# Performance work log

Hardware: AMD Instinct MI355X
Metric: run time of the kernel (lower is better)

## Reference

```python
import jax, jax.numpy as jnp
import numpy as np

N = 50000      # num_nodes
E = 800000     # num_edges (before self-loops)
IN = 512       # in_channels
HID = 64       # hidden_channels
H = 8          # num_heads (layer 1)
OUT = 128      # out_channels
NEG_SLOPE = 0.2


def setup_inputs() -> dict:
    key = jax.random.key(0)
    ks = jax.random.split(key, 10)
    x = jax.random.normal(ks[0], (N, IN), jnp.float32)
    edge_index = jax.random.randint(ks[1], (2, E), 0, N, jnp.int32)

    def glorot(k, shape):
        fan_in, fan_out = shape[0], int(np.prod(shape[1:]))
        s = jnp.sqrt(2.0 / (fan_in + fan_out)).astype(jnp.float32)
        return jax.random.normal(k, shape, jnp.float32) * s

    # layer 1: GATConv(IN -> HID, heads=H, concat=True)
    W1 = glorot(ks[2], (IN, H * HID))
    att_src1 = glorot(ks[3], (H, HID))
    att_dst1 = glorot(ks[4], (H, HID))
    b1 = jnp.zeros((H * HID,), jnp.float32)
    # layer 2: GATConv(H*HID -> OUT, heads=1, concat=False)
    W2 = glorot(ks[5], (H * HID, OUT))
    att_src2 = glorot(ks[6], (1, OUT))
    att_dst2 = glorot(ks[7], (1, OUT))
    b2 = jnp.zeros((OUT,), jnp.float32)
    return {"x": x, "edge_index": edge_index,
            "W1": W1, "b1": b1, "att_src1": att_src1, "att_dst1": att_dst1,
            "W2": W2, "b2": b2, "att_src2": att_src2, "att_dst2": att_dst2}


def gat_layer(x, src, dst, W, b, a_src, a_dst, heads, concat):
    n = x.shape[0]
    h = (x @ W).reshape(n, heads, -1)                     # [N, H, C]
    e_src = (h * a_src).sum(-1)                           # [N, H]
    e_dst = (h * a_dst).sum(-1)                           # [N, H]
    e = jax.nn.leaky_relu(e_src[src] + e_dst[dst], NEG_SLOPE)   # [E, H]
    # segment softmax over incoming edges of each destination node
    m = jax.ops.segment_max(e, dst, num_segments=n)       # [N, H]
    m = jnp.where(jnp.isneginf(m), 0.0, m)                # empty segments
    p = jnp.exp(e - m[dst])                               # [E, H]
    s = jax.ops.segment_sum(p, dst, num_segments=n)       # [N, H]
    alpha = p / (s[dst] + 1e-16)                          # [E, H]
    out = jax.ops.segment_sum(alpha[..., None] * h[src], dst, num_segments=n)  # [N, H, C]
    if concat:
        return out.reshape(n, -1) + b
    return out.mean(axis=1) + b


def reference(x, edge_index, W1, b1, att_src1, att_dst1, W2, b2, att_src2, att_dst2):
    # PyG GATConv adds self-loops by default
    loops = jnp.arange(N, dtype=edge_index.dtype)
    src = jnp.concatenate([edge_index[0], loops])
    dst = jnp.concatenate([edge_index[1], loops])
    h = gat_layer(x, src, dst, W1, b1, att_src1, att_dst1, H, True)   # [N, H*HID]
    h = jax.nn.relu(h)
    out = gat_layer(h, src, dst, W2, b2, att_src2, att_dst2, 1, False)  # [N, OUT]
    return out
```

## Files before the change

### kernel.cpp

```cpp
#include <hip/hip_runtime.h>

#define NNODES 50000
#define NEDGES 800000
#define ETOT   (NNODES + NEDGES)
#define NH     8
#define HID    64
#define D1     512
#define INC    512
#define OUTC   128
#define NEG    0.2f
#define MPAD   50048

typedef __attribute__((ext_vector_type(8))) short short8;
typedef __attribute__((ext_vector_type(4))) float f32x4;

__device__ __forceinline__ float bf2f(ushort u) { return __uint_as_float(((uint)u) << 16); }
__device__ __forceinline__ ushort f2bf(float x) {
    uint u = __float_as_uint(x);
    u += 0x7fffu + ((u >> 16) & 1u);
    return (ushort)(u >> 16);
}
__device__ __forceinline__ float leaky(float v) { return v >= 0.f ? v : NEG * v; }
__device__ __forceinline__ unsigned fkey(float v) {
    unsigned u = __float_as_uint(v);
    return (u & 0x80000000u) ? ~u : (u | 0x80000000u);
}
__device__ __forceinline__ float funkey(unsigned k) {
    return __uint_as_float((k & 0x80000000u) ? (k & 0x7fffffffu) : ~k);
}

__global__ void count_deg(const int* __restrict__ ei, int* __restrict__ deg) {
    int i = blockIdx.x * 256 + threadIdx.x;
    if (i >= ETOT) return;
    int dst = (i < NEDGES) ? ei[NEDGES + i] : (i - NEDGES);
    atomicAdd(&deg[dst], 1);
}

__global__ void scan_deg(const int* __restrict__ deg, int* __restrict__ rs) {
    __shared__ int part[1024];
    const int n = NNODES;
    const int CH = (n + 1023) / 1024;
    int t = threadIdx.x;
    int lo = t * CH, hi = min(lo + CH, n);
    int s = 0;
    for (int i = lo; i < hi; ++i) s += deg[i];
    part[t] = s;
    __syncthreads();
    for (int off = 1; off < 1024; off <<= 1) {
        int v = (t >= off) ? part[t - off] : 0;
        __syncthreads();
        part[t] += v;
        __syncthreads();
    }
    int run = (t == 0) ? 0 : part[t - 1];
    for (int i = lo; i < hi; ++i) { rs[i] = run; run += deg[i]; }
    if (hi == n) rs[n] = run;
}

__global__ void scatter_edges(const int* __restrict__ ei, int* __restrict__ cursor,
                              int* __restrict__ csr_src) {
    int i = blockIdx.x * 256 + threadIdx.x;
    if (i >= ETOT) return;
    int src, dst;
    if (i < NEDGES) { src = ei[i]; dst = ei[NEDGES + i]; }
    else            { src = dst = i - NEDGES; }
    int pos = atomicAdd(&cursor[dst], 1);
    csr_src[pos] = src;
}

__global__ void cast_bf16(const float* __restrict__ x, ushort* __restrict__ xb, int n4) {
    int i = blockIdx.x * 256 + threadIdx.x;
    if (i >= n4) return;
    float4 v = *(const float4*)&x[(size_t)i * 4];
    ushort4 o = { f2bf(v.x), f2bf(v.y), f2bf(v.z), f2bf(v.w) };
    *(ushort4*)&xb[(size_t)i * 4] = o;
}

__global__ void cast_wT(const float* __restrict__ W, ushort* __restrict__ WT, int K, int N) {
    int idx = blockIdx.x * 256 + threadIdx.x;
    if (idx >= K * N) return;
    int n = idx / K, k = idx - n * K;
    WT[idx] = f2bf(W[(size_t)k * N + n]);
}

template<int KDIM>
__global__ __launch_bounds__(256) void gemm_bf16(const ushort* __restrict__ A,
                                                 const ushort* __restrict__ Bt,
                                                 ushort* __restrict__ C,
                                                 int M, int N) {
    __shared__ __align__(16) ushort Asl[128 * 64];
    __shared__ __align__(16) ushort Bsl[128 * 64];
    const int tid  = threadIdx.x;
    const int lane = tid & 63;
    const int wid  = tid >> 6;
    const int wr   = wid >> 1, wc = wid & 1;
    const int fr   = lane & 15, fq = lane >> 4;
    const int m0   = blockIdx.x * 128;
    const int n0   = blockIdx.y * 128;

    f32x4 acc[4][4] = {};

    for (int k0 = 0; k0 < KDIM; k0 += 64) {
        __syncthreads();
        #pragma unroll
        for (int i = 0; i < 4; ++i) {
            int chunk = wid * 4 + i;
            int r = chunk * 8 + (lane >> 3);
            const ushort* ga = A  + (size_t)(m0 + r) * KDIM + k0 + (lane & 7) * 8;
            const ushort* gb = Bt + (size_t)(n0 + r) * KDIM + k0 + (lane & 7) * 8;
            __builtin_amdgcn_global_load_lds(
                (const __attribute__((address_space(1))) void*)ga,
                (__attribute__((address_space(3))) void*)(Asl + chunk * 512), 16, 0, 0);
            __builtin_amdgcn_global_load_lds(
                (const __attribute__((address_space(1))) void*)gb,
                (__attribute__((address_space(3))) void*)(Bsl + chunk * 512), 16, 0, 0);
        }
        __syncthreads();
        #pragma unroll
        for (int ks = 0; ks < 2; ++ks) {
            short8 a[4], b[4];
            #pragma unroll
            for (int m = 0; m < 4; ++m)
                a[m] = *(const short8*)&Asl[(wr * 64 + m * 16 + fr) * 64 + ks * 32 + fq * 8];
            #pragma unroll
            for (int n = 0; n < 4; ++n)
                b[n] = *(const short8*)&Bsl[(wc * 64 + n * 16 + fr) * 64 + ks * 32 + fq * 8];
            #pragma unroll
            for (int m = 0; m < 4; ++m)
                #pragma unroll
                for (int n = 0; n < 4; ++n)
                    acc[m][n] = __builtin_amdgcn_mfma_f32_16x16x32_bf16(a[m], b[n], acc[m][n], 0, 0, 0);
        }
    }
    #pragma unroll
    for (int m = 0; m < 4; ++m) {
        #pragma unroll
        for (int r = 0; r < 4; ++r) {
            int row = m0 + wr * 64 + m * 16 + fq * 4 + r;
            if (row >= M) continue;
            #pragma unroll
            for (int n = 0; n < 4; ++n)
                C[(size_t)row * N + n0 + wc * 64 + n * 16 + fr] = f2bf(acc[m][n][r]);
        }
    }
}

__global__ void dots1(const ushort* __restrict__ h1, const float* __restrict__ a_src,
                      const float* __restrict__ a_dst,
                      float* __restrict__ es, float* __restrict__ ed) {
    int gw   = (blockIdx.x * blockDim.x + threadIdx.x) >> 6;
    int lane = threadIdx.x & 63;
    if (gw >= NNODES) return;
    short8 v = *(const short8*)&h1[(size_t)gw * D1 + lane * 8];
    int h = lane >> 3, c0 = (lane & 7) * 8;
    float s = 0.f, d = 0.f;
    #pragma unroll
    for (int j = 0; j < 8; ++j) {
        float x = bf2f((ushort)v[j]);
        s += x * a_src[h * HID + c0 + j];
        d += x * a_dst[h * HID + c0 + j];
    }
    #pragma unroll
    for (int off = 1; off < 8; off <<= 1) {
        s += __shfl_xor(s, off);
        d += __shfl_xor(d, off);
    }
    if ((lane & 7) == 0) { es[gw * NH + h] = s; ed[gw * NH + h] = d; }
}

__global__ void dots2(const ushort* __restrict__ h2, const float* __restrict__ a_src,
                      const float* __restrict__ a_dst,
                      float* __restrict__ es, float* __restrict__ ed) {
    int gw   = (blockIdx.x * blockDim.x + threadIdx.x) >> 6;
    int lane = threadIdx.x & 63;
    if (gw >= NNODES) return;
    uint u = *(const uint*)&h2[(size_t)gw * OUTC + lane * 2];
    float x0 = bf2f((ushort)(u & 0xffffu)), x1 = bf2f((ushort)(u >> 16));
    float s = x0 * a_src[lane * 2] + x1 * a_src[lane * 2 + 1];
    float d = x0 * a_dst[lane * 2] + x1 * a_dst[lane * 2 + 1];
    #pragma unroll
    for (int off = 1; off < 64; off <<= 1) {
        s += __shfl_xor(s, off);
        d += __shfl_xor(d, off);
    }
    if (lane == 0) { es[gw] = s; ed[gw] = d; }
}

#define CAP1 128
__global__ __launch_bounds__(256) void attn1(const ushort* __restrict__ h1,
                                             const float* __restrict__ esrc,
                                             const float* __restrict__ edst,
                                             const int* __restrict__ rs,
                                             const int* __restrict__ csr_src,
                                             const float* __restrict__ b1,
                                             ushort* __restrict__ out1) {
    int n = blockIdx.x;
    int t = threadIdx.x;
    int beg = rs[n], deg = rs[n + 1] - beg;
    __shared__ float alpha_sh[CAP1][NH];
    __shared__ unsigned mkey[NH];
    __shared__ float msh[NH], ssh[NH], rinv[NH];
    if (t < NH) { mkey[t] = 0u; ssh[t] = 0.f; }
    __syncthreads();
    for (int idx = t; idx < deg * NH; idx += 256) {
        int e = idx >> 3, h = idx & 7;
        int s = csr_src[beg + e];
        float v = leaky(esrc[s * NH + h] + edst[n * NH + h]);
        atomicMax(&mkey[h], fkey(v));
        if (e < CAP1) alpha_sh[e][h] = v;
    }
    __syncthreads();
    if (t < NH) msh[t] = funkey(mkey[t]);
    __syncthreads();
    for (int idx = t; idx < deg * NH; idx += 256) {
        int e = idx >> 3, h = idx & 7;
        float v;
        if (e < CAP1) v = alpha_sh[e][h];
        else {
            int s = csr_src[beg + e];
            v = leaky(esrc[s * NH + h] + edst[n * NH + h]);
        }
        float p = __expf(v - msh[h]);
        atomicAdd(&ssh[h], p);
        if (e < CAP1) alpha_sh[e][h] = p;
    }
    __syncthreads();
    if (t < NH) rinv[t] = 1.f / (ssh[t] + 1e-16f);
    __syncthreads();
    int c0 = 2 * t;
    int h = t >> 5;
    float m = msh[h], ri = rinv[h], edn = edst[n * NH + h];
    float acc0 = 0.f, acc1 = 0.f;
    for (int e = 0; e < deg; ++e) {
        int s = csr_src[beg + e];
        float a;
        if (e < CAP1) a = alpha_sh[e][h];
        else          a = __expf(leaky(esrc[s * NH + h] + edn) - m);
        uint u = *(const uint*)&h1[(size_t)s * D1 + c0];
        acc0 += a * bf2f((ushort)(u & 0xffffu));
        acc1 += a * bf2f((ushort)(u >> 16));
    }
    float o0 = fmaxf(acc0 * ri + b1[c0], 0.f);
    float o1 = fmaxf(acc1 * ri + b1[c0 + 1], 0.f);
    uint pk = (uint)f2bf(o0) | ((uint)f2bf(o1) << 16);
    *(uint*)&out1[(size_t)n * D1 + c0] = pk;
}

#define CAP2 128
__global__ __launch_bounds__(128) void attn2(const ushort* __restrict__ h2,
                                             const float* __restrict__ esrc,
                                             const float* __restrict__ edst,
                                             const int* __restrict__ rs,
                                             const int* __restrict__ csr_src,
                                             const float* __restrict__ b2,
                                             float* __restrict__ out) {
    int n = blockIdx.x;
    int t = threadIdx.x;
    int beg = rs[n], deg = rs[n + 1] - beg;
    __shared__ float alpha_sh[CAP2];
    __shared__ unsigned mkey;
    __shared__ float msh, ssh, rinv;
    if (t == 0) { mkey = 0u; ssh = 0.f; }
    __syncthreads();
    float edn = edst[n];
    for (int e = t; e < deg; e += 128) {
        int s = csr_src[beg + e];
        float v = leaky(esrc[s] + edn);
        atomicMax(&mkey, fkey(v));
        if (e < CAP2) alpha_sh[e] = v;
    }
    __syncthreads();
    if (t == 0) msh = funkey(mkey);
    __syncthreads();
    for (int e = t; e < deg; e += 128) {
        float v;
        if (e < CAP2) v = alpha_sh[e];
        else { int s = csr_src[beg + e]; v = leaky(esrc[s] + edn); }
        float p = __expf(v - msh);
        atomicAdd(&ssh, p);
        if (e < CAP2) alpha_sh[e] = p;
    }
    __syncthreads();
    if (t == 0) rinv = 1.f / (ssh + 1e-16f);
    __syncthreads();
    float m = msh, ri = rinv;
    float acc = 0.f;
    for (int e = 0; e < deg; ++e) {
        int s = csr_src[beg + e];
        float a = (e < CAP2) ? alpha_sh[e] : __expf(leaky(esrc[s] + edn) - m);
        acc += a * bf2f(h2[(size_t)s * OUTC + t]);
    }
    out[(size_t)n * OUTC + t] = acc * ri + b2[t];
}

extern "C" void kernel_launch(void* const* d_in, const int* in_sizes, int n_in,
                              void* d_out, int out_size, void* d_ws, size_t ws_size,
                              hipStream_t stream) {
    const float* x   = (const float*)d_in[0];
    const int*   ei  = (const int*)  d_in[1];
    const float* W1  = (const float*)d_in[2];
    const float* b1  = (const float*)d_in[3];
    const float* as1 = (const float*)d_in[4];
    const float* ad1 = (const float*)d_in[5];
    const float* W2  = (const float*)d_in[6];
    const float* b2  = (const float*)d_in[7];
    const float* as2 = (const float*)d_in[8];
    const float* ad2 = (const float*)d_in[9];
    float* out = (float*)d_out;

    char* ws = (char*)d_ws;
    size_t off = 0;
    auto alloc = [&](size_t bytes) -> void* {
        void* p = ws + off;
        off = (off + bytes + 255) & ~(size_t)255;
        return p;
    };
    ushort* xb    = (ushort*)alloc((size_t)MPAD * INC * 2);
    ushort* w1t   = (ushort*)alloc((size_t)D1 * INC * 2);
    ushort* w2t   = (ushort*)alloc((size_t)OUTC * D1 * 2);
    ushort* h1b   = (ushort*)alloc((size_t)MPAD * D1 * 2);
    ushort* out1b = (ushort*)alloc((size_t)MPAD * D1 * 2);
    ushort* h2b   = (ushort*)alloc((size_t)MPAD * OUTC * 2);
    float*  es1   = (float*)alloc((size_t)NNODES * NH * 4);
    float*  ed1   = (float*)alloc((size_t)NNODES * NH * 4);
    float*  es2   = (float*)alloc((size_t)NNODES * 4);
    float*  ed2   = (float*)alloc((size_t)NNODES * 4);
    int*    deg   = (int*)alloc((size_t)NNODES * 4);
    int*    rs    = (int*)alloc((size_t)(NNODES + 1) * 4);
    int*    cur   = (int*)alloc((size_t)NNODES * 4);
    int*    csr   = (int*)alloc((size_t)ETOT * 4);

    hipMemsetAsync(deg, 0, (size_t)NNODES * 4, stream);
    count_deg<<<(ETOT + 255) / 256, 256, 0, stream>>>(ei, deg);
    scan_deg<<<1, 1024, 0, stream>>>(deg, rs);
    hipMemcpyAsync(cur, rs, (size_t)NNODES * 4, hipMemcpyDeviceToDevice, stream);
    scatter_edges<<<(ETOT + 255) / 256, 256, 0, stream>>>(ei, cur, csr);

    cast_bf16<<<(NNODES * INC / 4 + 255) / 256, 256, 0, stream>>>(x, xb, NNODES * INC / 4);
    cast_wT<<<(INC * D1 + 255) / 256, 256, 0, stream>>>(W1, w1t, INC, D1);
    cast_wT<<<(D1 * OUTC + 255) / 256, 256, 0, stream>>>(W2, w2t, D1, OUTC);

    gemm_bf16<INC><<<dim3(MPAD / 128, D1 / 128), 256, 0, stream>>>(xb, w1t, h1b, NNODES, D1);
    dots1<<<(NNODES * 64 + 255) / 256, 256, 0, stream>>>(h1b, as1, ad1, es1, ed1);
    attn1<<<NNODES, 256, 0, stream>>>(h1b, es1, ed1, rs, csr, b1, out1b);

    gemm_bf16<D1><<<dim3(MPAD / 128, OUTC / 128), 256, 0, stream>>>(out1b, w2t, h2b, NNODES, OUTC);
    dots2<<<(NNODES * 64 + 255) / 256, 256, 0, stream>>>(h2b, as2, ad2, es2, ed2);
    attn2<<<NNODES, 128, 0, stream>>>(h2b, es2, ed2, rs, csr, b2, out);
}
```

Measured before the change: 673.2 us.

## Replace shared-memory atomics in GAT softmax with wave-level reductions

Both attention kernels drop the shared-memory atomicMax/atomicAdd softmax and compute the max and sum with wavefront shuffle reductions; in attn1 each wave handles two heads. Source indices are staged in shared memory, and the aggregation loop is unrolled by four to put more gathers in flight. attn2 now assigns one wave per node, with four nodes per 256-thread block and two channels per lane. The aim is to remove atomic contention and barriers and to raise memory-level parallelism, at the cost of more shared memory and more code.

```diff
diff --git a/kernel.cpp b/kernel.cpp
--- a/kernel.cpp
+++ b/kernel.cpp
@@ -21,13 +21,6 @@
     return (ushort)(u >> 16);
 }
 __device__ __forceinline__ float leaky(float v) { return v >= 0.f ? v : NEG * v; }
-__device__ __forceinline__ unsigned fkey(float v) {
-    unsigned u = __float_as_uint(v);
-    return (u & 0x80000000u) ? ~u : (u | 0x80000000u);
-}
-__device__ __forceinline__ float funkey(unsigned k) {
-    return __uint_as_float((k & 0x80000000u) ? (k & 0x7fffffffu) : ~k);
-}
 
 __global__ void count_deg(const int* __restrict__ ei, int* __restrict__ deg) {
     int i = blockIdx.x * 256 + threadIdx.x;
@@ -196,46 +189,87 @@
                                              ushort* __restrict__ out1) {
     int n = blockIdx.x;
     int t = threadIdx.x;
+    int lane = t & 63, wid = t >> 6;
     int beg = rs[n], deg = rs[n + 1] - beg;
-    __shared__ float alpha_sh[CAP1][NH];
-    __shared__ unsigned mkey[NH];
-    __shared__ float msh[NH], ssh[NH], rinv[NH];
-    if (t < NH) { mkey[t] = 0u; ssh[t] = 0.f; }
+    int dcap = min(deg, CAP1);
+    __shared__ float alpha_sh[NH][CAP1];
+    __shared__ int   ssrc_sh[CAP1];
+    __shared__ float msh[NH], rinv_sh[NH];
+
+    for (int e = t; e < dcap; e += 256) ssrc_sh[e] = csr_src[beg + e];
     __syncthreads();
-    for (int idx = t; idx < deg * NH; idx += 256) {
-        int e = idx >> 3, h = idx & 7;
-        int s = csr_src[beg + e];
-        float v = leaky(esrc[s * NH + h] + edst[n * NH + h]);
-        atomicMax(&mkey[h], fkey(v));
-        if (e < CAP1) alpha_sh[e][h] = v;
+
+    {
+        int h0 = wid * 2;
+        float edn0 = edst[n * NH + h0], edn1 = edst[n * NH + h0 + 1];
+        float m0 = -1e30f, m1 = -1e30f;
+        for (int e = lane; e < deg; e += 64) {
+            int s = (e < CAP1) ? ssrc_sh[e] : csr_src[beg + e];
+            float2 es2 = *(const float2*)&esrc[s * NH + h0];
+            float v0 = leaky(es2.x + edn0), v1 = leaky(es2.y + edn1);
+            if (e < CAP1) { alpha_sh[h0][e] = v0; alpha_sh[h0 + 1][e] = v1; }
+            m0 = fmaxf(m0, v0); m1 = fmaxf(m1, v1);
+        }
+        #pragma unroll
+        for (int off = 32; off; off >>= 1) {
+            m0 = fmaxf(m0, __shfl_xor(m0, off));
+            m1 = fmaxf(m1, __shfl_xor(m1, off));
+        }
+        float s0 = 0.f, s1 = 0.f;
+        for (int e = lane; e < deg; e += 64) {
+            float v0, v1;
+            if (e < CAP1) { v0 = alpha_sh[h0][e]; v1 = alpha_sh[h0 + 1][e]; }
+            else {
+                int s = csr_src[beg + e];
+                float2 es2 = *(const float2*)&esrc[s * NH + h0];
+                v0 = leaky(es2.x + edn0); v1 = leaky(es2.y + edn1);
+            }
+            float p0 = __expf(v0 - m0), p1 = __expf(v1 - m1);
+            if (e < CAP1) { alpha_sh[h0][e] = p0; alpha_sh[h0 + 1][e] = p1; }
+            s0 += p0; s1 += p1;
+        }
+        #pragma unroll
+        for (int off = 32; off; off >>= 1) {
+            s0 += __shfl_xor(s0, off);
+            s1 += __shfl_xor(s1, off);
+        }
+        if (lane == 0) {
+            msh[h0] = m0; msh[h0 + 1] = m1;
+            rinv_sh[h0] = 1.f / (s0 + 1e-16f);
+            rinv_sh[h0 + 1] = 1.f / (s1 + 1e-16f);
+        }
     }
     __syncthreads();
-    if (t < NH) msh[t] = funkey(mkey[t]);
-    __syncthreads();
-    for (int idx = t; idx < deg * NH; idx += 256) {
-        int e = idx >> 3, h = idx & 7;
-        float v;
-        if (e < CAP1) v = alpha_sh[e][h];
-        else {
-            int s = csr_src[beg + e];
-            v = leaky(esrc[s * NH + h] + edst[n * NH + h]);
-        }
-        float p = __expf(v - msh[h]);
-        atomicAdd(&ssh[h], p);
-        if (e < CAP1) alpha_sh[e][h] = p;
-    }
-    __syncthreads();
-    if (t < NH) rinv[t] = 1.f / (ssh[t] + 1e-16f);
-    __syncthreads();
+
     int c0 = 2 * t;
     int h = t >> 5;
-    float m = msh[h], ri = rinv[h], edn = edst[n * NH + h];
+    float m = msh[h], ri = rinv_sh[h];
+    float edn = edst[n * NH + h];
     float acc0 = 0.f, acc1 = 0.f;
-    for (int e = 0; e < deg; ++e) {
+    int e = 0;
+    for (; e + 4 <= dcap; e += 4) {
+        int s0i = ssrc_sh[e], s1i = ssrc_sh[e + 1], s2i = ssrc_sh[e + 2], s3i = ssrc_sh[e + 3];
+        uint u0 = *(const uint*)&h1[(size_t)s0i * D1 + c0];
+        uint u1 = *(const uint*)&h1[(size_t)s1i * D1 + c0];
+        uint u2 = *(const uint*)&h1[(size_t)s2i * D1 + c0];
+        uint u3 = *(const uint*)&h1[(size_t)s3i * D1 + c0];
+        float a0 = alpha_sh[h][e], a1 = alpha_sh[h][e + 1];
+        float a2 = alpha_sh[h][e + 2], a3 = alpha_sh[h][e + 3];
+        acc0 += a0 * bf2f((ushort)(u0 & 0xffffu)) + a1 * bf2f((ushort)(u1 & 0xffffu))
+              + a2 * bf2f((ushort)(u2 & 0xffffu)) + a3 * bf2f((ushort)(u3 & 0xffffu));
+        acc1 += a0 * bf2f((ushort)(u0 >> 16)) + a1 * bf2f((ushort)(u1 >> 16))
+              + a2 * bf2f((ushort)(u2 >> 16)) + a3 * bf2f((ushort)(u3 >> 16));
+    }
+    for (; e < dcap; ++e) {
+        int s = ssrc_sh[e];
+        float a = alpha_sh[h][e];
+        uint u = *(const uint*)&h1[(size_t)s * D1 + c0];
+        acc0 += a * bf2f((ushort)(u & 0xffffu));
+        acc1 += a * bf2f((ushort)(u >> 16));
+    }
+    for (; e < deg; ++e) {
         int s = csr_src[beg + e];
-        float a;
-        if (e < CAP1) a = alpha_sh[e][h];
-        else          a = __expf(leaky(esrc[s * NH + h] + edn) - m);
+        float a = __expf(leaky(esrc[s * NH + h] + edn) - m);
         uint u = *(const uint*)&h1[(size_t)s * D1 + c0];
         acc0 += a * bf2f((ushort)(u & 0xffffu));
         acc1 += a * bf2f((ushort)(u >> 16));
@@ -247,50 +281,77 @@
 }
 
 #define CAP2 128
-__global__ __launch_bounds__(128) void attn2(const ushort* __restrict__ h2,
+__global__ __launch_bounds__(256) void attn2(const ushort* __restrict__ h2,
                                              const float* __restrict__ esrc,
                                              const float* __restrict__ edst,
                                              const int* __restrict__ rs,
                                              const int* __restrict__ csr_src,
                                              const float* __restrict__ b2,
                                              float* __restrict__ out) {
-    int n = blockIdx.x;
-    int t = threadIdx.x;
+    int lane = threadIdx.x & 63, wid = threadIdx.x >> 6;
+    int n = blockIdx.x * 4 + wid;
+    if (n >= NNODES) return;
     int beg = rs[n], deg = rs[n + 1] - beg;
-    __shared__ float alpha_sh[CAP2];
-    __shared__ unsigned mkey;
-    __shared__ float msh, ssh, rinv;
-    if (t == 0) { mkey = 0u; ssh = 0.f; }
-    __syncthreads();
+    int dcap = min(deg, CAP2);
+    __shared__ float al_sh[4][CAP2];
+    __shared__ int   ss_sh[4][CAP2];
+    float* al = al_sh[wid];
+    int*   ss = ss_sh[wid];
+
+    for (int e = lane; e < dcap; e += 64) ss[e] = csr_src[beg + e];
+
     float edn = edst[n];
-    for (int e = t; e < deg; e += 128) {
+    float m = -1e30f;
+    for (int e = lane; e < deg; e += 64) {
+        int s = (e < CAP2) ? ss[e] : csr_src[beg + e];
+        float v = leaky(esrc[s] + edn);
+        if (e < CAP2) al[e] = v;
+        m = fmaxf(m, v);
+    }
+    #pragma unroll
+    for (int off = 32; off; off >>= 1) m = fmaxf(m, __shfl_xor(m, off));
+    float ssum = 0.f;
+    for (int e = lane; e < deg; e += 64) {
+        float v = (e < CAP2) ? al[e] : leaky(esrc[csr_src[beg + e]] + edn);
+        float p = __expf(v - m);
+        if (e < CAP2) al[e] = p;
+        ssum += p;
+    }
+    #pragma unroll
+    for (int off = 32; off; off >>= 1) ssum += __shfl_xor(ssum, off);
+    float ri = 1.f / (ssum + 1e-16f);
+
+    int c0 = 2 * lane;
+    float acc0 = 0.f, acc1 = 0.f;
+    int e = 0;
+    for (; e + 4 <= dcap; e += 4) {
+        int s0i = ss[e], s1i = ss[e + 1], s2i = ss[e + 2], s3i = ss[e + 3];
+        uint u0 = *(const uint*)&h2[(size_t)s0i * OUTC + c0];
+        uint u1 = *(const uint*)&h2[(size_t)s1i * OUTC + c0];
+        uint u2 = *(const uint*)&h2[(size_t)s2i * OUTC + c0];
+        uint u3 = *(const uint*)&h2[(size_t)s3i * OUTC + c0];
+        float a0 = al[e], a1 = al[e + 1], a2 = al[e + 2], a3 = al[e + 3];
+        acc0 += a0 * bf2f((ushort)(u0 & 0xffffu)) + a1 * bf2f((ushort)(u1 & 0xffffu))
+              + a2 * bf2f((ushort)(u2 & 0xffffu)) + a3 * bf2f((ushort)(u3 & 0xffffu));
+        acc1 += a0 * bf2f((ushort)(u0 >> 16)) + a1 * bf2f((ushort)(u1 >> 16))
+              + a2 * bf2f((ushort)(u2 >> 16)) + a3 * bf2f((ushort)(u3 >> 16));
+    }
+    for (; e < dcap; ++e) {
+        int s = ss[e];
+        float a = al[e];
+        uint u = *(const uint*)&h2[(size_t)s * OUTC + c0];
+        acc0 += a * bf2f((ushort)(u & 0xffffu));
+        acc1 += a * bf2f((ushort)(u >> 16));
+    }
+    for (; e < deg; ++e) {
         int s = csr_src[beg + e];
-        float v = leaky(esrc[s] + edn);
-        atomicMax(&mkey, fkey(v));
-        if (e < CAP2) alpha_sh[e] = v;
-    }
-    __syncthreads();
-    if (t == 0) msh = funkey(mkey);
-    __syncthreads();
-    for (int e = t; e < deg; e += 128) {
-        float v;
-        if (e < CAP2) v = alpha_sh[e];
-        else { int s = csr_src[beg + e]; v = leaky(esrc[s] + edn); }
-        float p = __expf(v - msh);
-        atomicAdd(&ssh, p);
-        if (e < CAP2) alpha_sh[e] = p;
-    }
-    __syncthreads();
-    if (t == 0) rinv = 1.f / (ssh + 1e-16f);
-    __syncthreads();
-    float m = msh, ri = rinv;
-    float acc = 0.f;
-    for (int e = 0; e < deg; ++e) {
-        int s = csr_src[beg + e];
-        float a = (e < CAP2) ? alpha_sh[e] : __expf(leaky(esrc[s] + edn) - m);
-        acc += a * bf2f(h2[(size_t)s * OUTC + t]);
-    }
-    out[(size_t)n * OUTC + t] = acc * ri + b2[t];
+        float a = __expf(leaky(esrc[s] + edn) - m);
+        uint u = *(const uint*)&h2[(size_t)s * OUTC + c0];
+        acc0 += a * bf2f((ushort)(u & 0xffffu));
+        acc1 += a * bf2f((ushort)(u >> 16));
+    }
+    float2 o = { acc0 * ri + b2[c0], acc1 * ri + b2[c0 + 1] };
+    *(float2*)&out[(size_t)n * OUTC + c0] = o;
 }
 
 extern "C" void kernel_launch(void* const* d_in, const int* in_sizes, int n_in,
@@ -346,5 +407,5 @@
 
     gemm_bf16<D1><<<dim3(MPAD / 128, OUTC / 128), 256, 0, stream>>>(out1b, w2t, h2b, NNODES, OUTC);
     dots2<<<(NNODES * 64 + 255) / 256, 256, 0, stream>>>(h2b, as2, ad2, es2, ed2);
-    attn2<<<NNODES, 128, 0, stream>>>(h2b, es2, ed2, rs, csr, b2, out);
-}
+    attn2<<<(NNODES + 3) / 4, 256, 0, stream>>>(h2b, es2, ed2, rs, csr, b2, out);
+}
```

Result: faster. 611.4 us (-9.2%).
